# Performance work log

Hardware: AMD Instinct MI355X
Metric: run time of the kernel (lower is better)

## Reference

```python
import jax, jax.numpy as jnp
import numpy as np

V = 32000   # vocab_size
E = 512     # embed_size
H = 512     # hidden_size
T = 64      # encoder seq len
B = 16      # batch


def setup_inputs() -> dict:
    key = jax.random.key(0)
    ks = jax.random.split(key, 18)
    s = 0.05
    return {
        "u_enc_out": jax.random.normal(ks[0], (T, B, H), jnp.float32),
        "a_tm1": jax.random.randint(ks[1], (1, B), 0, V),
        "last_hidden": jax.random.normal(ks[2], (1, B, H), jnp.float32),
        "u_input_np": jax.random.randint(ks[3], (T, B), 0, V),
        "sparse_u_input": jax.random.uniform(ks[4], (B, T, V + T), jnp.float32),
        # learned parameters
        "emb": jax.random.normal(ks[5], (V, E), jnp.float32) * s,
        "W_ih": jax.random.normal(ks[6], (3 * H, E + H), jnp.float32) * s,
        "b_ih": jnp.zeros((3 * H,), jnp.float32),
        "W_hh": jax.random.normal(ks[7], (3 * H, H), jnp.float32) * s,
        "b_hh": jnp.zeros((3 * H,), jnp.float32),
        "proj_W": jax.random.normal(ks[8], (V, 2 * H), jnp.float32) * s,
        "proj_b": jnp.zeros((V,), jnp.float32),
        "attn_W": jax.random.normal(ks[9], (H, 2 * H), jnp.float32) * s,
        "attn_b": jnp.zeros((H,), jnp.float32),
        "attn_v": jax.random.normal(ks[10], (H,), jnp.float32) * (1.0 / np.sqrt(H)),
        "copy_W": jax.random.normal(ks[11], (H, H), jnp.float32) * s,
        "copy_b": jnp.zeros((H,), jnp.float32),
    }


def reference(u_enc_out, a_tm1, last_hidden, u_input_np, sparse_u_input,
              emb, W_ih, b_ih, W_hh, b_hh, proj_W, proj_b,
              attn_W, attn_b, attn_v, copy_W, copy_b):
    # ---- Bahdanau attention over encoder outputs (mask path is dead in source) ----
    enc = jnp.transpose(u_enc_out, (1, 0, 2))            # [B,T,H]
    h0 = last_hidden[0]                                   # [B,H]
    Hrep = jnp.broadcast_to(h0[:, None, :], enc.shape)    # [B,T,H]
    energy = jnp.tanh(jnp.concatenate([Hrep, enc], -1) @ attn_W.T + attn_b)  # [B,T,H]
    attn_e = jnp.einsum('bth,h->bt', energy, attn_v)      # [B,T]
    alpha = jax.nn.softmax(attn_e, axis=-1)
    context = jnp.einsum('bt,bth->bh', alpha, enc)        # [B,H]

    # ---- one GRU step (PyTorch gate order: r, z, n) ----
    x = jnp.concatenate([emb[a_tm1[0]], context], -1)     # [B,E+H]
    gx = x @ W_ih.T + b_ih
    gh = h0 @ W_hh.T + b_hh
    xr, xz, xn = jnp.split(gx, 3, -1)
    hr, hz, hn = jnp.split(gh, 3, -1)
    r = jax.nn.sigmoid(xr + hr)
    z = jax.nn.sigmoid(xz + hz)
    n = jnp.tanh(xn + r * hn)
    h1 = (1.0 - z) * n + z * h0                           # [B,H]
    gru_out = h1[None]                                    # [1,B,H]

    # ---- generation scores ----
    gen_score = jnp.concatenate([h1, context], -1) @ proj_W.T + proj_b  # [B,V]

    # ---- copy scores with stable exp/log-sum trick ----
    ucs = jnp.tanh(enc @ copy_W.T + copy_b)               # [B,T,H]
    ucs = jnp.einsum('bth,bh->bt', ucs, h1)               # [B,T]
    m = jnp.max(ucs, axis=1, keepdims=True)
    ucs = jnp.exp(ucs - m)
    ucs = jnp.log(jnp.einsum('bt,btv->bv', ucs, sparse_u_input)) + m    # [B,V+T]

    # ---- combined softmax over [gen | copy] ----
    scores = jax.nn.softmax(jnp.concatenate([gen_score, ucs], 1), axis=1)
    gen = scores[:, :V]
    cp = scores[:, V:]                                    # [B,V+T]
    proba = jnp.concatenate([gen + cp[:, :V], cp[:, V:]], 1)
    return (gru_out, h1[None], proba)
```

## Files before the change

### kernel.cpp

```cpp
#include <hip/hip_runtime.h>
#include <hip/hip_bf16.h>
#include <math.h>

#define V_SZ 32000
#define E_SZ 512
#define H_SZ 512
#define T_SZ 64
#define B_SZ 16
#define VT_SZ (V_SZ + T_SZ)
#define TOT_SM (V_SZ + VT_SZ)

#define WS_H0ATT 0u
#define WS_GH    8192u
#define WS_E1    32768u
#define WS_TANHC 557056u
#define WS_EATTN 1081344u
#define WS_X     1082368u
#define WS_GX    1098752u
#define WS_Y     1123328u
#define WS_WT    1139712u
#define WS_MB    1140736u
#define WS_PART  1140752u
#define WS_GL    3188752u
#define WS_UCSV  3700752u

__device__ __forceinline__ float dot4(float4 a, float4 b) {
    return fmaf(a.x, b.x, fmaf(a.y, b.y, fmaf(a.z, b.z, a.w * b.w)));
}

__global__ __launch_bounds__(256) void k_prep(const float* __restrict__ last_hidden,
        const float* __restrict__ attn_W, const float* __restrict__ attn_b,
        const float* __restrict__ W_hh, const float* __restrict__ b_hh,
        float* __restrict__ ws) {
    int i = blockIdx.x * 256 + threadIdx.x;
    int b = i >> 11, j = i & 2047;
    const float* h0 = last_hidden + b * H_SZ;
    if (j < 512) {
        const float* wr = attn_W + j * 1024;
        float acc = attn_b[j];
        for (int k = 0; k < 512; k += 4)
            acc += dot4(*(const float4*)(h0 + k), *(const float4*)(wr + k));
        ws[WS_H0ATT + b * 512 + j] = acc;
    } else {
        int jj = j - 512;
        const float* wr = W_hh + jj * 512;
        float acc = b_hh[jj];
        for (int k = 0; k < 512; k += 4)
            acc += dot4(*(const float4*)(h0 + k), *(const float4*)(wr + k));
        ws[WS_GH + b * 1536 + jj] = acc;
    }
}

__global__ __launch_bounds__(256) void k_encgemm(const float* __restrict__ u,
        const float* __restrict__ attn_W, const float* __restrict__ copy_W,
        const float* __restrict__ copy_b, float* __restrict__ ws) {
    __shared__ float As[64][33];
    __shared__ float Bs[64][33];
    float* E1 = ws + WS_E1;
    float* tanhC = ws + WS_TANHC;
    int bx = blockIdx.x, by = blockIdx.y;
    int tid = threadIdx.x;
    int tm = tid & 15, tn = tid >> 4;
    float acc[4][4] = {};
    int r = tid >> 3;
    int c4 = (tid & 7) * 4;
    for (int k0 = 0; k0 < 512; k0 += 32) {
        #pragma unroll
        for (int rep = 0; rep < 2; ++rep) {
            int rr = r + rep * 32;
            float4 av = *(const float4*)(u + (rr * 16 + by) * 512 + k0 + c4);
            As[rr][c4 + 0] = av.x; As[rr][c4 + 1] = av.y;
            As[rr][c4 + 2] = av.z; As[rr][c4 + 3] = av.w;
            const float* brow = (bx < 8) ? (attn_W + (bx * 64 + rr) * 1024 + 512)
                                         : (copy_W + ((bx - 8) * 64 + rr) * 512);
            float4 bv = *(const float4*)(brow + k0 + c4);
            Bs[rr][c4 + 0] = bv.x; Bs[rr][c4 + 1] = bv.y;
            Bs[rr][c4 + 2] = bv.z; Bs[rr][c4 + 3] = bv.w;
        }
        __syncthreads();
        #pragma unroll 8
        for (int kk = 0; kk < 32; ++kk) {
            float a0 = As[tm * 4 + 0][kk], a1 = As[tm * 4 + 1][kk];
            float a2 = As[tm * 4 + 2][kk], a3 = As[tm * 4 + 3][kk];
            float b0 = Bs[tn * 4 + 0][kk], b1 = Bs[tn * 4 + 1][kk];
            float b2 = Bs[tn * 4 + 2][kk], b3 = Bs[tn * 4 + 3][kk];
            acc[0][0] = fmaf(a0, b0, acc[0][0]); acc[0][1] = fmaf(a0, b1, acc[0][1]);
            acc[0][2] = fmaf(a0, b2, acc[0][2]); acc[0][3] = fmaf(a0, b3, acc[0][3]);
            acc[1][0] = fmaf(a1, b0, acc[1][0]); acc[1][1] = fmaf(a1, b1, acc[1][1]);
            acc[1][2] = fmaf(a1, b2, acc[1][2]); acc[1][3] = fmaf(a1, b3, acc[1][3]);
            acc[2][0] = fmaf(a2, b0, acc[2][0]); acc[2][1] = fmaf(a2, b1, acc[2][1]);
            acc[2][2] = fmaf(a2, b2, acc[2][2]); acc[2][3] = fmaf(a2, b3, acc[2][3]);
            acc[3][0] = fmaf(a3, b0, acc[3][0]); acc[3][1] = fmaf(a3, b1, acc[3][1]);
            acc[3][2] = fmaf(a3, b2, acc[3][2]); acc[3][3] = fmaf(a3, b3, acc[3][3]);
        }
        __syncthreads();
    }
    #pragma unroll
    for (int i = 0; i < 4; ++i) {
        int t = tm * 4 + i;
        #pragma unroll
        for (int j = 0; j < 4; ++j) {
            int c = tn * 4 + j;
            if (bx < 8) {
                E1[(by * 64 + t) * 512 + bx * 64 + c] = acc[i][j];
            } else {
                int n2 = (bx - 8) * 64 + c;
                tanhC[(by * 64 + t) * 512 + n2] = tanhf(acc[i][j] + copy_b[n2]);
            }
        }
    }
}

__global__ __launch_bounds__(256) void k_attn_e(const float* __restrict__ attn_v,
        float* __restrict__ ws) {
    int b = blockIdx.x, tchunk = blockIdx.y;
    int t = tchunk * 8 + (threadIdx.x >> 5);
    int lane = threadIdx.x & 31;
    const float* h0att = ws + WS_H0ATT + b * 512;
    const float* e1 = ws + WS_E1 + (b * 64 + t) * 512;
    float s = 0.f;
    #pragma unroll
    for (int i = 0; i < 16; ++i) {
        int h = lane + 32 * i;
        s += tanhf(h0att[h] + e1[h]) * attn_v[h];
    }
    #pragma unroll
    for (int m = 16; m >= 1; m >>= 1) s += __shfl_xor(s, m);
    if (lane == 0) ws[WS_EATTN + b * 64 + t] = s;
}

__global__ __launch_bounds__(256) void k_attn_ctx(const float* __restrict__ u,
        const int* __restrict__ a_tm1, const float* __restrict__ emb,
        float* __restrict__ ws) {
    int b = blockIdx.x, tid = threadIdx.x;
    __shared__ float alpha[64];
    if (tid < 64) {
        float v = ws[WS_EATTN + b * 64 + tid];
        float m = v;
        #pragma unroll
        for (int k = 32; k >= 1; k >>= 1) m = fmaxf(m, __shfl_xor(m, k));
        float ex = expf(v - m);
        float s = ex;
        #pragma unroll
        for (int k = 32; k >= 1; k >>= 1) s += __shfl_xor(s, k);
        alpha[tid] = ex / s;
    }
    __syncthreads();
    int a = a_tm1[b];
    float* x = ws + WS_X + b * 1024;
    for (int h = tid; h < 512; h += 256) {
        float ctx = 0.f;
        #pragma unroll 8
        for (int t = 0; t < 64; ++t) ctx += alpha[t] * u[(t * 16 + b) * 512 + h];
        x[512 + h] = ctx;
        x[h] = emb[a * 512 + h];
    }
}

__global__ __launch_bounds__(256) void k_gx(const float* __restrict__ W_ih,
        const float* __restrict__ b_ih, float* __restrict__ ws) {
    int j = blockIdx.x * 16 + (threadIdx.x >> 4);
    int b = threadIdx.x & 15;
    const float* xr = ws + WS_X + b * 1024;
    const float* wr = W_ih + j * 1024;
    float acc = b_ih[j];
    for (int k = 0; k < 1024; k += 4)
        acc += dot4(*(const float4*)(xr + k), *(const float4*)(wr + k));
    ws[WS_GX + b * 1536 + j] = acc;
}

__global__ __launch_bounds__(256) void k_h1(const float* __restrict__ last_hidden,
        float* __restrict__ ws, float* __restrict__ out) {
    int i = blockIdx.x * 256 + threadIdx.x;
    int b = i >> 9, h = i & 511;
    const float* gx = ws + WS_GX + b * 1536;
    const float* gh = ws + WS_GH + b * 1536;
    float r = 1.f / (1.f + expf(-(gx[h] + gh[h])));
    float z = 1.f / (1.f + expf(-(gx[512 + h] + gh[512 + h])));
    float n = tanhf(gx[1024 + h] + r * gh[1024 + h]);
    float h0v = last_hidden[b * 512 + h];
    float h1 = (1.f - z) * n + z * h0v;
    out[i] = h1;
    out[8192 + i] = h1;
    ws[WS_Y + b * 1024 + h] = h1;
    ws[WS_Y + b * 1024 + 512 + h] = ws[WS_X + b * 1024 + 512 + h];
}

__global__ __launch_bounds__(256) void k_gen(const float* __restrict__ proj_W,
        float* __restrict__ ws) {
    __shared__ float ys[16][256];
    int kq = blockIdx.y, tid = threadIdx.x;
    for (int i = tid; i < 4096; i += 256) {
        int b = i >> 8, c = i & 255;
        ys[b][c] = ws[WS_Y + b * 1024 + kq * 256 + c];
    }
    __syncthreads();
    int v0 = blockIdx.x * 512 + tid;
    int v1 = v0 + 256;
    bool g1 = v1 < V_SZ;
    float acc0[16] = {}, acc1[16] = {};
    const float* w0p = proj_W + (size_t)v0 * 1024 + kq * 256;
    const float* w1p = proj_W + (size_t)v1 * 1024 + kq * 256;
    for (int c = 0; c < 256; c += 4) {
        float4 w0 = *(const float4*)(w0p + c);
        float4 w1 = g1 ? *(const float4*)(w1p + c) : make_float4(0.f, 0.f, 0.f, 0.f);
        #pragma unroll
        for (int b = 0; b < 16; ++b) {
            float4 yv = *(const float4*)(&ys[b][c]);
            acc0[b] = fmaf(w0.x, yv.x, fmaf(w0.y, yv.y, fmaf(w0.z, yv.z, fmaf(w0.w, yv.w, acc0[b]))));
            acc1[b] = fmaf(w1.x, yv.x, fmaf(w1.y, yv.y, fmaf(w1.z, yv.z, fmaf(w1.w, yv.w, acc1[b]))));
        }
    }
    float* part = ws + WS_PART;
    #pragma unroll
    for (int b = 0; b < 16; ++b) {
        part[(size_t)(kq * 16 + b) * V_SZ + v0] = acc0[b];
        if (g1) part[(size_t)(kq * 16 + b) * V_SZ + v1] = acc1[b];
    }
}

__global__ __launch_bounds__(256) void k_genred(const float* __restrict__ proj_b,
        float* __restrict__ ws) {
    int idx = blockIdx.x * 256 + threadIdx.x;
    int b = idx / V_SZ, v = idx - b * V_SZ;
    const float* part = ws + WS_PART;
    float g = proj_b[v];
    #pragma unroll
    for (int kq = 0; kq < 4; ++kq) g += part[(size_t)(kq * 16 + b) * V_SZ + v];
    ws[WS_GL + (size_t)b * V_SZ + v] = g;
}

__global__ __launch_bounds__(256) void k_copyscore(float* __restrict__ ws) {
    int b = blockIdx.x, tid = threadIdx.x;
    int t = tid >> 2, q = tid & 3;
    const float* tc = ws + WS_TANHC + (b * 64 + t) * 512;
    const float* h1 = ws + WS_Y + b * 1024;
    float s = 0.f;
    for (int i = 0; i < 128; i += 4) {
        int h = q * 128 + i;
        s += dot4(*(const float4*)(tc + h), *(const float4*)(h1 + h));
    }
    s += __shfl_xor(s, 1);
    s += __shfl_xor(s, 2);
    __shared__ float uc[64];
    if (q == 0) uc[t] = s;
    __syncthreads();
    if (tid < 64) {
        float v = uc[tid];
        float m = v;
        #pragma unroll
        for (int k = 32; k >= 1; k >>= 1) m = fmaxf(m, __shfl_xor(m, k));
        ws[WS_WT + b * 64 + tid] = expf(v - m);
        if (tid == 0) ws[WS_MB + b] = m;
    }
}

__global__ __launch_bounds__(256) void k_ucsv(const float* __restrict__ sparse,
        float* __restrict__ ws) {
    int b = blockIdx.y;
    int v = blockIdx.x * 256 + threadIdx.x;
    __shared__ float wsm[64];
    if (threadIdx.x < 64) wsm[threadIdx.x] = ws[WS_WT + b * 64 + threadIdx.x];
    __syncthreads();
    if (v >= VT_SZ) return;
    const float* sp = sparse + (size_t)b * 64 * VT_SZ + v;
    float acc = 0.f;
    #pragma unroll 8
    for (int t = 0; t < 64; ++t) acc = fmaf(wsm[t], sp[(size_t)t * VT_SZ], acc);
    ws[WS_UCSV + (size_t)b * VT_SZ + v] = logf(acc) + ws[WS_MB + b];
}

__global__ __launch_bounds__(1024) void k_final(float* __restrict__ ws, float* __restrict__ out) {
    int b = blockIdx.x, tid = threadIdx.x;
    const float* gl = ws + WS_GL + (size_t)b * V_SZ;
    const float* uv = ws + WS_UCSV + (size_t)b * VT_SZ;
    __shared__ float red[16];
    float m = -3.0e38f;
    for (int i = tid; i < TOT_SM; i += 1024) {
        float v = (i < V_SZ) ? gl[i] : uv[i - V_SZ];
        m = fmaxf(m, v);
    }
    #pragma unroll
    for (int k = 32; k >= 1; k >>= 1) m = fmaxf(m, __shfl_xor(m, k));
    if ((tid & 63) == 0) red[tid >> 6] = m;
    __syncthreads();
    float M = red[0];
    #pragma unroll
    for (int i = 1; i < 16; ++i) M = fmaxf(M, red[i]);
    __syncthreads();
    float s = 0.f;
    for (int i = tid; i < TOT_SM; i += 1024) {
        float v = (i < V_SZ) ? gl[i] : uv[i - V_SZ];
        s += expf(v - M);
    }
    #pragma unroll
    for (int k = 32; k >= 1; k >>= 1) s += __shfl_xor(s, k);
    if ((tid & 63) == 0) red[tid >> 6] = s;
    __syncthreads();
    float S = 0.f;
    #pragma unroll
    for (int i = 0; i < 16; ++i) S += red[i];
    float invS = 1.f / S;
    float* ob = out + 16384 + (size_t)b * VT_SZ;
    for (int i = tid; i < VT_SZ; i += 1024) {
        float cp = expf(uv[i] - M) * invS;
        float p = (i < V_SZ) ? fmaf(expf(gl[i] - M), invS, cp) : cp;
        ob[i] = p;
    }
}

extern "C" void kernel_launch(void* const* d_in, const int* in_sizes, int n_in,
                              void* d_out, int out_size, void* d_ws, size_t ws_size,
                              hipStream_t stream) {
    (void)in_sizes; (void)n_in; (void)out_size; (void)ws_size;
    const float* u_enc   = (const float*)d_in[0];
    const int*   a_tm1   = (const int*)d_in[1];
    const float* last_h  = (const float*)d_in[2];
    const float* sparse  = (const float*)d_in[4];
    const float* emb     = (const float*)d_in[5];
    const float* W_ih    = (const float*)d_in[6];
    const float* b_ih    = (const float*)d_in[7];
    const float* W_hh    = (const float*)d_in[8];
    const float* b_hh    = (const float*)d_in[9];
    const float* proj_W  = (const float*)d_in[10];
    const float* proj_b  = (const float*)d_in[11];
    const float* attn_W  = (const float*)d_in[12];
    const float* attn_b  = (const float*)d_in[13];
    const float* attn_v  = (const float*)d_in[14];
    const float* copy_W  = (const float*)d_in[15];
    const float* copy_b  = (const float*)d_in[16];
    float* ws  = (float*)d_ws;
    float* out = (float*)d_out;

    hipLaunchKernelGGL(k_prep, dim3(128), dim3(256), 0, stream,
                       last_h, attn_W, attn_b, W_hh, b_hh, ws);
    hipLaunchKernelGGL(k_encgemm, dim3(16, 16), dim3(256), 0, stream,
                       u_enc, attn_W, copy_W, copy_b, ws);
    hipLaunchKernelGGL(k_attn_e, dim3(16, 8), dim3(256), 0, stream, attn_v, ws);
    hipLaunchKernelGGL(k_attn_ctx, dim3(16), dim3(256), 0, stream, u_enc, a_tm1, emb, ws);
    hipLaunchKernelGGL(k_gx, dim3(96), dim3(256), 0, stream, W_ih, b_ih, ws);
    hipLaunchKernelGGL(k_h1, dim3(32), dim3(256), 0, stream, last_h, ws, out);
    hipLaunchKernelGGL(k_gen, dim3(63, 4), dim3(256), 0, stream, proj_W, ws);
    hipLaunchKernelGGL(k_genred, dim3(2000), dim3(256), 0, stream, proj_b, ws);
    hipLaunchKernelGGL(k_copyscore, dim3(16), dim3(256), 0, stream, ws);
    hipLaunchKernelGGL(k_ucsv, dim3(126, 16), dim3(256), 0, stream, sparse, ws);
    hipLaunchKernelGGL(k_final, dim3(16), dim3(1024), 0, stream, ws, out);
}
```

Before: 533.7 us.

## Use wave-level coalesced GEMV for projections and split final softmax across blocks

Adds a shared wave-level GEMV helper in which each wave handles 16 weight rows across all 16 batches, with lanes splitting K and results reduced through shuffles. It is used for the attention/GRU prep GEMVs, the input-gate GEMV and the vocab projection, which removes the split-K partials buffer and the separate reduce kernel. The copy-score sparse product and the final softmax write are vectorised to float4. The final softmax is split into an 8-chunk-per-batch statistics pass plus a wide parallel write kernel, replacing the previous 16-block reduction. In exchange the GEMVs hold large per-thread accumulator arrays, which raises register pressure, and the final stage adds a kernel launch.

```diff
diff --git a/kernel.cpp b/kernel.cpp
--- a/kernel.cpp
+++ b/kernel.cpp
@@ -20,7 +20,7 @@
 #define WS_Y     1123328u
 #define WS_WT    1139712u
 #define WS_MB    1140736u
-#define WS_PART  1140752u
+#define WS_FST   1140752u
 #define WS_GL    3188752u
 #define WS_UCSV  3700752u
 
@@ -28,26 +28,93 @@
     return fmaf(a.x, b.x, fmaf(a.y, b.y, fmaf(a.z, b.z, a.w * b.w)));
 }
 
-__global__ __launch_bounds__(256) void k_prep(const float* __restrict__ last_hidden,
+template<int NPASS>
+__device__ __forceinline__ void wave_gemv16(
+        const float* __restrict__ W,
+        int ldw,
+        const float* __restrict__ y,
+        int ldy,
+        const float* __restrict__ bias,
+        float* __restrict__ out, int ostride, int rowglob) {
+    int lane = threadIdx.x & 63;
+    int ks = lane & 15, s = lane >> 4;
+    float acc[16][4];
+    #pragma unroll
+    for (int r = 0; r < 16; ++r)
+        #pragma unroll
+        for (int n = 0; n < 4; ++n) acc[r][n] = 0.f;
+
+    for (int p = 0; p < NPASS; ++p) {
+        int kk = ks * 4 + p * 64;
+        float4 y4[4];
+        #pragma unroll
+        for (int n = 0; n < 4; ++n)
+            y4[n] = *(const float4*)(y + (4 * s + n) * ldy + kk);
+        #pragma unroll
+        for (int r = 0; r < 16; ++r) {
+            float4 w4 = *(const float4*)(W + r * ldw + kk);
+            #pragma unroll
+            for (int n = 0; n < 4; ++n)
+                acc[r][n] = fmaf(w4.x, y4[n].x, fmaf(w4.y, y4[n].y,
+                            fmaf(w4.z, y4[n].z, fmaf(w4.w, y4[n].w, acc[r][n]))));
+        }
+    }
+    float a8[8][4];
+    #pragma unroll
+    for (int r = 0; r < 8; ++r)
+        #pragma unroll
+        for (int n = 0; n < 4; ++n) {
+            float keep = (lane & 8) ? acc[r + 8][n] : acc[r][n];
+            float send = (lane & 8) ? acc[r][n] : acc[r + 8][n];
+            a8[r][n] = keep + __shfl_xor(send, 8);
+        }
+    float a4_[4][4];
+    #pragma unroll
+    for (int r = 0; r < 4; ++r)
+        #pragma unroll
+        for (int n = 0; n < 4; ++n) {
+            float keep = (lane & 4) ? a8[r + 4][n] : a8[r][n];
+            float send = (lane & 4) ? a8[r][n] : a8[r + 4][n];
+            a4_[r][n] = keep + __shfl_xor(send, 4);
+        }
+    float a2_[2][4];
+    #pragma unroll
+    for (int r = 0; r < 2; ++r)
+        #pragma unroll
+        for (int n = 0; n < 4; ++n) {
+            float keep = (lane & 2) ? a4_[r + 2][n] : a4_[r][n];
+            float send = (lane & 2) ? a4_[r][n] : a4_[r + 2][n];
+            a2_[r][n] = keep + __shfl_xor(send, 2);
+        }
+    float a1_[4];
+    #pragma unroll
+    for (int n = 0; n < 4; ++n) {
+        float keep = (lane & 1) ? a2_[1][n] : a2_[0][n];
+        float send = (lane & 1) ? a2_[0][n] : a2_[1][n];
+        a1_[n] = keep + __shfl_xor(send, 1);
+    }
+    int rf = lane & 15;
+    float bv = bias[rf];
+    #pragma unroll
+    for (int n = 0; n < 4; ++n)
+        out[(size_t)(4 * s + n) * ostride + rowglob + rf] = a1_[n] + bv;
+}
+
+__global__ __launch_bounds__(256) void k_prep2(const float* __restrict__ last_hidden,
         const float* __restrict__ attn_W, const float* __restrict__ attn_b,
         const float* __restrict__ W_hh, const float* __restrict__ b_hh,
         float* __restrict__ ws) {
-    int i = blockIdx.x * 256 + threadIdx.x;
-    int b = i >> 11, j = i & 2047;
-    const float* h0 = last_hidden + b * H_SZ;
-    if (j < 512) {
-        const float* wr = attn_W + j * 1024;
-        float acc = attn_b[j];
-        for (int k = 0; k < 512; k += 4)
-            acc += dot4(*(const float4*)(h0 + k), *(const float4*)(wr + k));
-        ws[WS_H0ATT + b * 512 + j] = acc;
+    int gw = blockIdx.x * 4 + (threadIdx.x >> 6);
+    int rowbase = gw * 16;
+    if (rowbase < 512) {
+        wave_gemv16<8>(attn_W + (size_t)rowbase * 1024, 1024,
+                       last_hidden, 512, attn_b + rowbase,
+                       ws + WS_H0ATT, 512, rowbase);
     } else {
-        int jj = j - 512;
-        const float* wr = W_hh + jj * 512;
-        float acc = b_hh[jj];
-        for (int k = 0; k < 512; k += 4)
-            acc += dot4(*(const float4*)(h0 + k), *(const float4*)(wr + k));
-        ws[WS_GH + b * 1536 + jj] = acc;
+        int r2 = rowbase - 512;
+        wave_gemv16<8>(W_hh + (size_t)r2 * 512, 512,
+                       last_hidden, 512, b_hh + r2,
+                       ws + WS_GH, 1536, r2);
     }
 }
 
@@ -157,16 +224,13 @@
     }
 }
 
-__global__ __launch_bounds__(256) void k_gx(const float* __restrict__ W_ih,
+__global__ __launch_bounds__(256) void k_gx2(const float* __restrict__ W_ih,
         const float* __restrict__ b_ih, float* __restrict__ ws) {
-    int j = blockIdx.x * 16 + (threadIdx.x >> 4);
-    int b = threadIdx.x & 15;
-    const float* xr = ws + WS_X + b * 1024;
-    const float* wr = W_ih + j * 1024;
-    float acc = b_ih[j];
-    for (int k = 0; k < 1024; k += 4)
-        acc += dot4(*(const float4*)(xr + k), *(const float4*)(wr + k));
-    ws[WS_GX + b * 1536 + j] = acc;
+    int gw = blockIdx.x * 4 + (threadIdx.x >> 6);
+    int rowbase = gw * 16;
+    wave_gemv16<16>(W_ih + (size_t)rowbase * 1024, 1024,
+                    ws + WS_X, 1024, b_ih + rowbase,
+                    ws + WS_GX, 1536, rowbase);
 }
 
 __global__ __launch_bounds__(256) void k_h1(const float* __restrict__ last_hidden,
@@ -186,48 +250,13 @@
     ws[WS_Y + b * 1024 + 512 + h] = ws[WS_X + b * 1024 + 512 + h];
 }
 
-__global__ __launch_bounds__(256) void k_gen(const float* __restrict__ proj_W,
-        float* __restrict__ ws) {
-    __shared__ float ys[16][256];
-    int kq = blockIdx.y, tid = threadIdx.x;
-    for (int i = tid; i < 4096; i += 256) {
-        int b = i >> 8, c = i & 255;
-        ys[b][c] = ws[WS_Y + b * 1024 + kq * 256 + c];
-    }
-    __syncthreads();
-    int v0 = blockIdx.x * 512 + tid;
-    int v1 = v0 + 256;
-    bool g1 = v1 < V_SZ;
-    float acc0[16] = {}, acc1[16] = {};
-    const float* w0p = proj_W + (size_t)v0 * 1024 + kq * 256;
-    const float* w1p = proj_W + (size_t)v1 * 1024 + kq * 256;
-    for (int c = 0; c < 256; c += 4) {
-        float4 w0 = *(const float4*)(w0p + c);
-        float4 w1 = g1 ? *(const float4*)(w1p + c) : make_float4(0.f, 0.f, 0.f, 0.f);
-        #pragma unroll
-        for (int b = 0; b < 16; ++b) {
-            float4 yv = *(const float4*)(&ys[b][c]);
-            acc0[b] = fmaf(w0.x, yv.x, fmaf(w0.y, yv.y, fmaf(w0.z, yv.z, fmaf(w0.w, yv.w, acc0[b]))));
-            acc1[b] = fmaf(w1.x, yv.x, fmaf(w1.y, yv.y, fmaf(w1.z, yv.z, fmaf(w1.w, yv.w, acc1[b]))));
-        }
-    }
-    float* part = ws + WS_PART;
-    #pragma unroll
-    for (int b = 0; b < 16; ++b) {
-        part[(size_t)(kq * 16 + b) * V_SZ + v0] = acc0[b];
-        if (g1) part[(size_t)(kq * 16 + b) * V_SZ + v1] = acc1[b];
-    }
-}
-
-__global__ __launch_bounds__(256) void k_genred(const float* __restrict__ proj_b,
-        float* __restrict__ ws) {
-    int idx = blockIdx.x * 256 + threadIdx.x;
-    int b = idx / V_SZ, v = idx - b * V_SZ;
-    const float* part = ws + WS_PART;
-    float g = proj_b[v];
-    #pragma unroll
-    for (int kq = 0; kq < 4; ++kq) g += part[(size_t)(kq * 16 + b) * V_SZ + v];
-    ws[WS_GL + (size_t)b * V_SZ + v] = g;
+__global__ __launch_bounds__(256) void k_gen2(const float* __restrict__ proj_W,
+        const float* __restrict__ proj_b, float* __restrict__ ws) {
+    int gw = blockIdx.x * 4 + (threadIdx.x >> 6);
+    int rowbase = gw * 16;
+    wave_gemv16<16>(proj_W + (size_t)rowbase * 1024, 1024,
+                    ws + WS_Y, 1024, proj_b + rowbase,
+                    ws + WS_GL, V_SZ, rowbase);
 }
 
 __global__ __launch_bounds__(256) void k_copyscore(float* __restrict__ ws) {
@@ -258,38 +287,51 @@
 __global__ __launch_bounds__(256) void k_ucsv(const float* __restrict__ sparse,
         float* __restrict__ ws) {
     int b = blockIdx.y;
-    int v = blockIdx.x * 256 + threadIdx.x;
+    int v4 = (blockIdx.x * 256 + threadIdx.x) * 4;
     __shared__ float wsm[64];
     if (threadIdx.x < 64) wsm[threadIdx.x] = ws[WS_WT + b * 64 + threadIdx.x];
     __syncthreads();
-    if (v >= VT_SZ) return;
-    const float* sp = sparse + (size_t)b * 64 * VT_SZ + v;
-    float acc = 0.f;
-    #pragma unroll 8
-    for (int t = 0; t < 64; ++t) acc = fmaf(wsm[t], sp[(size_t)t * VT_SZ], acc);
-    ws[WS_UCSV + (size_t)b * VT_SZ + v] = logf(acc) + ws[WS_MB + b];
-}
-
-__global__ __launch_bounds__(1024) void k_final(float* __restrict__ ws, float* __restrict__ out) {
-    int b = blockIdx.x, tid = threadIdx.x;
+    if (v4 >= VT_SZ) return;
+    const float* sp = sparse + (size_t)b * 64 * VT_SZ + v4;
+    float4 acc = make_float4(0.f, 0.f, 0.f, 0.f);
+    #pragma unroll 4
+    for (int t = 0; t < 64; ++t) {
+        float w = wsm[t];
+        float4 s = *(const float4*)(sp + (size_t)t * VT_SZ);
+        acc.x = fmaf(w, s.x, acc.x);
+        acc.y = fmaf(w, s.y, acc.y);
+        acc.z = fmaf(w, s.z, acc.z);
+        acc.w = fmaf(w, s.w, acc.w);
+    }
+    float m = ws[WS_MB + b];
+    float4 r;
+    r.x = logf(acc.x) + m; r.y = logf(acc.y) + m;
+    r.z = logf(acc.z) + m; r.w = logf(acc.w) + m;
+    *(float4*)(ws + WS_UCSV + (size_t)b * VT_SZ + v4) = r;
+}
+
+__global__ __launch_bounds__(256) void k_fstat(float* __restrict__ ws) {
+    int b = blockIdx.x, c = blockIdx.y;
+    int tid = threadIdx.x;
     const float* gl = ws + WS_GL + (size_t)b * V_SZ;
     const float* uv = ws + WS_UCSV + (size_t)b * VT_SZ;
-    __shared__ float red[16];
+    int i0 = c * 8008, i1 = i0 + 8008;
     float m = -3.0e38f;
-    for (int i = tid; i < TOT_SM; i += 1024) {
+    for (int i = i0 + tid; i < i1; i += 256) {
         float v = (i < V_SZ) ? gl[i] : uv[i - V_SZ];
         m = fmaxf(m, v);
     }
     #pragma unroll
     for (int k = 32; k >= 1; k >>= 1) m = fmaxf(m, __shfl_xor(m, k));
+    __shared__ float red[4];
+    __shared__ float Msh;
     if ((tid & 63) == 0) red[tid >> 6] = m;
     __syncthreads();
-    float M = red[0];
-    #pragma unroll
-    for (int i = 1; i < 16; ++i) M = fmaxf(M, red[i]);
-    __syncthreads();
+    if (tid == 0) Msh = fmaxf(fmaxf(red[0], red[1]), fmaxf(red[2], red[3]));
+    __syncthreads();
+    float M = Msh;
     float s = 0.f;
-    for (int i = tid; i < TOT_SM; i += 1024) {
+    for (int i = i0 + tid; i < i1; i += 256) {
         float v = (i < V_SZ) ? gl[i] : uv[i - V_SZ];
         s += expf(v - M);
     }
@@ -297,16 +339,41 @@
     for (int k = 32; k >= 1; k >>= 1) s += __shfl_xor(s, k);
     if ((tid & 63) == 0) red[tid >> 6] = s;
     __syncthreads();
+    if (tid == 0) {
+        ws[WS_FST + (b * 8 + c) * 2 + 0] = M;
+        ws[WS_FST + (b * 8 + c) * 2 + 1] = red[0] + red[1] + red[2] + red[3];
+    }
+}
+
+__global__ __launch_bounds__(256) void k_fwrite(float* __restrict__ ws,
+        float* __restrict__ out) {
+    int b = blockIdx.y;
+    int i4 = (blockIdx.x * 256 + threadIdx.x) * 4;
+    const float* st = ws + WS_FST + b * 16;
+    float M = -3.0e38f;
+    #pragma unroll
+    for (int c = 0; c < 8; ++c) M = fmaxf(M, st[c * 2]);
     float S = 0.f;
     #pragma unroll
-    for (int i = 0; i < 16; ++i) S += red[i];
+    for (int c = 0; c < 8; ++c) S += st[c * 2 + 1] * expf(st[c * 2] - M);
     float invS = 1.f / S;
-    float* ob = out + 16384 + (size_t)b * VT_SZ;
-    for (int i = tid; i < VT_SZ; i += 1024) {
-        float cp = expf(uv[i] - M) * invS;
-        float p = (i < V_SZ) ? fmaf(expf(gl[i] - M), invS, cp) : cp;
-        ob[i] = p;
-    }
+    if (i4 >= VT_SZ) return;
+    const float* gl = ws + WS_GL + (size_t)b * V_SZ;
+    const float* uv = ws + WS_UCSV + (size_t)b * VT_SZ;
+    float4 u4 = *(const float4*)(uv + i4);
+    float4 r;
+    r.x = expf(u4.x - M) * invS;
+    r.y = expf(u4.y - M) * invS;
+    r.z = expf(u4.z - M) * invS;
+    r.w = expf(u4.w - M) * invS;
+    if (i4 < V_SZ) {
+        float4 g4 = *(const float4*)(gl + i4);
+        r.x += expf(g4.x - M) * invS;
+        r.y += expf(g4.y - M) * invS;
+        r.z += expf(g4.z - M) * invS;
+        r.w += expf(g4.w - M) * invS;
+    }
+    *(float4*)(out + 16384 + (size_t)b * VT_SZ + i4) = r;
 }
 
 extern "C" void kernel_launch(void* const* d_in, const int* in_sizes, int n_in,
@@ -332,17 +399,17 @@
     float* ws  = (float*)d_ws;
     float* out = (float*)d_out;
 
-    hipLaunchKernelGGL(k_prep, dim3(128), dim3(256), 0, stream,
+    hipLaunchKernelGGL(k_prep2, dim3(32), dim3(256), 0, stream,
                        last_h, attn_W, attn_b, W_hh, b_hh, ws);
     hipLaunchKernelGGL(k_encgemm, dim3(16, 16), dim3(256), 0, stream,
                        u_enc, attn_W, copy_W, copy_b, ws);
     hipLaunchKernelGGL(k_attn_e, dim3(16, 8), dim3(256), 0, stream, attn_v, ws);
     hipLaunchKernelGGL(k_attn_ctx, dim3(16), dim3(256), 0, stream, u_enc, a_tm1, emb, ws);
-    hipLaunchKernelGGL(k_gx, dim3(96), dim3(256), 0, stream, W_ih, b_ih, ws);
+    hipLaunchKernelGGL(k_gx2, dim3(24), dim3(256), 0, stream, W_ih, b_ih, ws);
     hipLaunchKernelGGL(k_h1, dim3(32), dim3(256), 0, stream, last_h, ws, out);
-    hipLaunchKernelGGL(k_gen, dim3(63, 4), dim3(256), 0, stream, proj_W, ws);
-    hipLaunchKernelGGL(k_genred, dim3(2000), dim3(256), 0, stream, proj_b, ws);
+    hipLaunchKernelGGL(k_gen2, dim3(500), dim3(256), 0, stream, proj_W, proj_b, ws);
     hipLaunchKernelGGL(k_copyscore, dim3(16), dim3(256), 0, stream, ws);
-    hipLaunchKernelGGL(k_ucsv, dim3(126, 16), dim3(256), 0, stream, sparse, ws);
-    hipLaunchKernelGGL(k_final, dim3(16), dim3(1024), 0, stream, ws, out);
-}
+    hipLaunchKernelGGL(k_ucsv, dim3(32, 16), dim3(256), 0, stream, sparse, ws);
+    hipLaunchKernelGGL(k_fstat, dim3(16, 8), dim3(256), 0, stream, ws);
+    hipLaunchKernelGGL(k_fwrite, dim3(32, 16), dim3(256), 0, stream, ws, out);
+}
```

Measured after the change: 497.1 us. 1.07x faster.
